# Kernel tuning notes

Hardware: AMD Instinct MI355X
Metric: run time of the kernel (lower is better)

Reference implementation:

```python
import jax, jax.numpy as jnp
import numpy as np

EPS = 1e-8  # torch cosine_similarity clamps norms at 1e-8
TEMPERATURE = 0.05


def _normalize(x):
    n = jnp.linalg.norm(x, axis=-1, keepdims=True)
    return x / jnp.maximum(n, EPS)


def setup_inputs() -> dict:
    key = jax.random.key(0)
    k1, k2, k3 = jax.random.split(key, 3)
    N, D = 8192, 256
    return {
        "text_embeddings": jax.random.normal(k1, (N, D), dtype=jnp.float32),
        "text_pos_embeddings": jax.random.normal(k2, (N, D), dtype=jnp.float32),
        "text_neg_embeddings": jax.random.normal(k3, (N, D), dtype=jnp.float32),
    }


def _pair_loss(a, b):
    # PairInBatchNegCoSentLoss(a, b): cos-sim matrix, scale, diag-subtract, LSE
    sim = _normalize(a) @ _normalize(b).T / TEMPERATURE  # [N, N]
    diff = sim - jnp.diagonal(sim)[:, None]
    return jax.nn.logsumexp(diff, axis=1).mean()


def reference(text_embeddings, text_pos_embeddings, text_neg_embeddings):
    e = _normalize(text_embeddings)
    p = _normalize(text_pos_embeddings)
    n = _normalize(text_neg_embeddings)
    sim_pos = jnp.sum(e * p, axis=-1)          # [N]
    sim_neg = e @ n.T                          # [N, N]
    sim = jnp.concatenate([sim_pos[:, None], sim_neg], axis=1) / TEMPERATURE
    diff = sim - sim[:, 0:1]
    loss = jax.nn.logsumexp(diff, axis=1).mean()
    # add_swap_loss=True: pair loss with (pos, anchor) swapped
    loss = loss + _pair_loss(text_pos_embeddings, text_embeddings)
    return loss
```

## Files before the change

### kernel.cpp

```cpp
#include <hip/hip_runtime.h>
#include <stdint.h>

#define N 8192
#define D 256
#define INV_T 20.0f
#define LOG2E 1.44269504088896340736f
#define BM 128
#define BN 128
#define NXB 64

typedef __attribute__((ext_vector_type(16))) float f32x16;
typedef __attribute__((ext_vector_type(4))) int i32x4;
typedef __attribute__((ext_vector_type(8))) int i32x8;

typedef __attribute__((address_space(3))) uint32_t lds_u32;
typedef __attribute__((address_space(1))) const uint32_t gbl_u32;

static __device__ __forceinline__ float fast_exp2(float x) {
  float r;
  asm("v_exp_f32 %0, %1" : "=v"(r) : "v"(x));
  return r;
}

__global__ __launch_bounds__(256) void normalize_kernel(
    const float* __restrict__ e, const float* __restrict__ p, const float* __restrict__ n,
    uint32_t* __restrict__ eb, uint32_t* __restrict__ pb, uint32_t* __restrict__ nb,
    float* __restrict__ cbuf, float* __restrict__ out) {
  const int tid = threadIdx.x;
  const int wave = tid >> 6, lane = tid & 63;
  const int row = blockIdx.x * 4 + wave;

  if (blockIdx.x == 0 && tid == 0) out[0] = 0.0f;

  const float4 ev = ((const float4*)(e + (size_t)row * D))[lane];
  const float4 pv = ((const float4*)(p + (size_t)row * D))[lane];
  const float4 nv = ((const float4*)(n + (size_t)row * D))[lane];

  float sse = ev.x*ev.x + ev.y*ev.y + ev.z*ev.z + ev.w*ev.w;
  float ssp = pv.x*pv.x + pv.y*pv.y + pv.z*pv.z + pv.w*pv.w;
  float ssn = nv.x*nv.x + nv.y*nv.y + nv.z*nv.z + nv.w*nv.w;
  float dep = ev.x*pv.x + ev.y*pv.y + ev.z*pv.z + ev.w*pv.w;
#pragma unroll
  for (int m = 1; m < 64; m <<= 1) {
    sse += __shfl_xor(sse, m);
    ssp += __shfl_xor(ssp, m);
    ssn += __shfl_xor(ssn, m);
    dep += __shfl_xor(dep, m);
  }
  const float se = 1.0f / fmaxf(sqrtf(sse), 1e-8f);
  const float sp = 1.0f / fmaxf(sqrtf(ssp), 1e-8f);
  const float sn = 1.0f / fmaxf(sqrtf(ssn), 1e-8f);

  int ue = __builtin_amdgcn_cvt_pk_fp8_f32(ev.x*se, ev.y*se, 0, false);
  ue     = __builtin_amdgcn_cvt_pk_fp8_f32(ev.z*se, ev.w*se, ue, true);
  int up = __builtin_amdgcn_cvt_pk_fp8_f32(pv.x*sp, pv.y*sp, 0, false);
  up     = __builtin_amdgcn_cvt_pk_fp8_f32(pv.z*sp, pv.w*sp, up, true);
  int un = __builtin_amdgcn_cvt_pk_fp8_f32(nv.x*sn, nv.y*sn, 0, false);
  un     = __builtin_amdgcn_cvt_pk_fp8_f32(nv.z*sn, nv.w*sn, un, true);
  eb[row * 64 + lane] = (uint32_t)ue;
  pb[row * 64 + lane] = (uint32_t)up;
  nb[row * 64 + lane] = (uint32_t)un;

  if (lane == 0) cbuf[row] = dep * se * sp * INV_T;
}

__global__ __launch_bounds__(256, 3) void simexp_kernel(
    const uint8_t* __restrict__ eb, const uint8_t* __restrict__ pb,
    const uint8_t* __restrict__ nb, const float* __restrict__ cbuf,
    float* __restrict__ part) {
  __shared__ uint8_t Bs[BN * D];

  const int z = blockIdx.z;
  const uint8_t* __restrict__ A = z ? pb : eb;
  const uint8_t* __restrict__ B = z ? eb : nb;

  const int tid = threadIdx.x;
  const int wave = tid >> 6, lane = tid & 63;
  const int lane31 = lane & 31, half = lane >> 5;
  const int rowTile = blockIdx.x * BM, colblk = blockIdx.y;
  const int colTile = colblk * BN;

#pragma unroll
  for (int i = 0; i < 8; ++i) {
    const int c = i * 256 + tid, r = c >> 4, sl = c & 15;
    const int gg = sl ^ (r & 15);
    __builtin_amdgcn_global_load_lds(
        (gbl_u32*)(B + (size_t)(colTile + r) * D + gg * 16),
        (lds_u32*)&Bs[c * 16], 16, 0, 0);
  }

  const int arow = rowTile + wave * 32 + lane31;
  const uint8_t* __restrict__ Arow = A + (size_t)arow * D + half * 32;
  i32x8 afr[4];
#pragma unroll
  for (int s = 0; s < 4; ++s) {
    const i32x4 lo = *(const i32x4*)(Arow + s * 64);
    const i32x4 hi = *(const i32x4*)(Arow + s * 64 + 16);
    afr[s] = (i32x8){lo[0], lo[1], lo[2], lo[3], hi[0], hi[1], hi[2], hi[3]};
  }

  const float cv = cbuf[arow] * LOG2E;

  int bbase[4];
#pragma unroll
  for (int ni = 0; ni < 4; ++ni) {
    const int cl = ni * 32 + lane31;
    bbase[ni] = (cl << 8) ^ ((cl & 15) << 4) ^ (half << 5);
  }

  f32x16 acc[4];
#pragma unroll
  for (int ni = 0; ni < 4; ++ni)
#pragma unroll
    for (int r = 0; r < 16; ++r) acc[ni][r] = 0.0f;

  __syncthreads();

#pragma unroll
  for (int s = 0; s < 4; ++s) {
#pragma unroll
    for (int ni = 0; ni < 4; ++ni) {
      const int alo = bbase[ni] ^ (s << 6);
      const i32x4 blo = *(const i32x4*)&Bs[alo];
      const i32x4 bhi = *(const i32x4*)&Bs[alo ^ 16];
      const i32x8 b = (i32x8){blo[0], blo[1], blo[2], blo[3],
                              bhi[0], bhi[1], bhi[2], bhi[3]};
      acc[ni] = __builtin_amdgcn_mfma_scale_f32_32x32x64_f8f6f4(
          b, afr[s], acc[ni],
          0 , 0 ,
          0, 0x7F7F7F7F , 0, 0x7F7F7F7F );
    }
  }

  const float K2 = INV_T * LOG2E;
  float sacc0 = 0.0f, sacc1 = 0.0f, sacc2 = 0.0f, sacc3 = 0.0f;
#pragma unroll
  for (int reg = 0; reg < 16; ++reg) {
    sacc0 += fast_exp2(acc[0][reg] * K2 - cv);
    sacc1 += fast_exp2(acc[1][reg] * K2 - cv);
    sacc2 += fast_exp2(acc[2][reg] * K2 - cv);
    sacc3 += fast_exp2(acc[3][reg] * K2 - cv);
  }
  float v = (sacc0 + sacc1) + (sacc2 + sacc3);
  v += __shfl_xor(v, 32);
  if (lane < 32)
    part[((size_t)(z * NXB + colblk)) * N + rowTile + wave * 32 + lane] = v;
}

__global__ __launch_bounds__(64) void finalize_kernel(const float* __restrict__ part,
                                                      float* __restrict__ out) {
  const int r = blockIdx.x * 64 + threadIdx.x;
  const int z = r >> 13, row = r & (N - 1);
  const float* __restrict__ base = part + (size_t)(z * NXB) * N + row;
  float s0 = 0.0f, s1 = 0.0f, s2 = 0.0f, s3 = 0.0f;
#pragma unroll
  for (int x = 0; x < NXB; x += 4) {
    s0 += base[(size_t)(x + 0) * N];
    s1 += base[(size_t)(x + 1) * N];
    s2 += base[(size_t)(x + 2) * N];
    s3 += base[(size_t)(x + 3) * N];
  }
  const float s = (s0 + s1) + (s2 + s3);
  float val = z ? logf(s) : log1pf(s);
#pragma unroll
  for (int m = 1; m < 64; m <<= 1) val += __shfl_xor(val, m);
  if (threadIdx.x == 0) atomicAdd(out, val * (1.0f / (float)N));
}

extern "C" void kernel_launch(void* const* d_in, const int* in_sizes, int n_in,
                              void* d_out, int out_size, void* d_ws, size_t ws_size,
                              hipStream_t stream) {
  const float* e = (const float*)d_in[0];
  const float* p = (const float*)d_in[1];
  const float* n = (const float*)d_in[2];

  char* w = (char*)d_ws;
  uint8_t* eb = (uint8_t*)w;
  uint8_t* pb = eb + (size_t)N * D;
  uint8_t* nb = pb + (size_t)N * D;
  float* cbuf = (float*)(nb + (size_t)N * D);
  float* part = cbuf + N;

  normalize_kernel<<<N / 4, 256, 0, stream>>>(e, p, n, (uint32_t*)eb, (uint32_t*)pb,
                                              (uint32_t*)nb, cbuf, (float*)d_out);
  simexp_kernel<<<dim3(N / BM, N / BN, 2), 256, 0, stream>>>(eb, pb, nb, cbuf, part);
  finalize_kernel<<<256, 64, 0, stream>>>(part, (float*)d_out);
}
```

Baseline: 134.1 us.

## Make simexp persistent over column tiles with double-buffered B staging

Each simexp block now keeps its A fragments in registers and loops over 16 consecutive 128-column B tiles. B tiles are double-buffered in LDS via async global-to-LDS loads, so the load of the next-but-one tile overlaps MFMA and exp work. This cuts the grid from 64x64x2 blocks to 4x64x2, amortizes A loads, and shrinks the partial-sum buffer and finalize reduction from 64 to 4 chunks. In exchange it doubles LDS use and lowers the occupancy hint from 3 to 2. The grid drops to 512 blocks, which may underfill the 256 CUs.

```diff
diff --git a/kernel.cpp b/kernel.cpp
--- a/kernel.cpp
+++ b/kernel.cpp
@@ -7,7 +7,8 @@
 #define LOG2E 1.44269504088896340736f
 #define BM 128
 #define BN 128
-#define NXB 64
+#define NCHUNK 4
+#define NT 16
 
 typedef __attribute__((ext_vector_type(16))) float f32x16;
 typedef __attribute__((ext_vector_type(4))) int i32x4;
@@ -64,11 +65,11 @@
   if (lane == 0) cbuf[row] = dep * se * sp * INV_T;
 }
 
-__global__ __launch_bounds__(256, 3) void simexp_kernel(
+__global__ __launch_bounds__(256, 2) void simexp_kernel(
     const uint8_t* __restrict__ eb, const uint8_t* __restrict__ pb,
     const uint8_t* __restrict__ nb, const float* __restrict__ cbuf,
     float* __restrict__ part) {
-  __shared__ uint8_t Bs[BN * D];
+  __shared__ uint8_t Bs[2][BN * D];
 
   const int z = blockIdx.z;
   const uint8_t* __restrict__ A = z ? pb : eb;
@@ -77,17 +78,21 @@
   const int tid = threadIdx.x;
   const int wave = tid >> 6, lane = tid & 63;
   const int lane31 = lane & 31, half = lane >> 5;
-  const int rowTile = blockIdx.x * BM, colblk = blockIdx.y;
-  const int colTile = colblk * BN;
-
-#pragma unroll
-  for (int i = 0; i < 8; ++i) {
-    const int c = i * 256 + tid, r = c >> 4, sl = c & 15;
-    const int gg = sl ^ (r & 15);
-    __builtin_amdgcn_global_load_lds(
-        (gbl_u32*)(B + (size_t)(colTile + r) * D + gg * 16),
-        (lds_u32*)&Bs[c * 16], 16, 0, 0);
-  }
+  const int chunk = blockIdx.x;
+  const int rowTile = blockIdx.y * BM;
+  const int colblk0 = chunk * NT;
+
+#define STAGEB(buf, cblk)                                                     \
+  do {                                                                        \
+    const uint8_t* __restrict__ Bsrc = B + (size_t)(cblk) * (BN * D);         \
+    _Pragma("unroll") for (int i = 0; i < 8; ++i) {                           \
+      const int c = i * 256 + tid, r = c >> 4, sl = c & 15;                   \
+      const int gg = sl ^ (r & 15);                                           \
+      __builtin_amdgcn_global_load_lds(                                       \
+          (gbl_u32*)(Bsrc + (size_t)r * D + gg * 16),                         \
+          (lds_u32*)&Bs[buf][c * 16], 16, 0, 0);                              \
+    }                                                                         \
+  } while (0)
 
   const int arow = rowTile + wave * 32 + lane31;
   const uint8_t* __restrict__ Arow = A + (size_t)arow * D + half * 32;
@@ -98,8 +103,11 @@
     const i32x4 hi = *(const i32x4*)(Arow + s * 64 + 16);
     afr[s] = (i32x8){lo[0], lo[1], lo[2], lo[3], hi[0], hi[1], hi[2], hi[3]};
   }
-
   const float cv = cbuf[arow] * LOG2E;
+  __builtin_amdgcn_sched_barrier(0);
+  STAGEB(0, colblk0 + 0);
+  STAGEB(1, colblk0 + 1);
+  __builtin_amdgcn_sched_barrier(0);
 
   int bbase[4];
 #pragma unroll
@@ -108,58 +116,70 @@
     bbase[ni] = (cl << 8) ^ ((cl & 15) << 4) ^ (half << 5);
   }
 
-  f32x16 acc[4];
-#pragma unroll
-  for (int ni = 0; ni < 4; ++ni)
-#pragma unroll
-    for (int r = 0; r < 16; ++r) acc[ni][r] = 0.0f;
-
-  __syncthreads();
-
-#pragma unroll
-  for (int s = 0; s < 4; ++s) {
-#pragma unroll
-    for (int ni = 0; ni < 4; ++ni) {
-      const int alo = bbase[ni] ^ (s << 6);
-      const i32x4 blo = *(const i32x4*)&Bs[alo];
-      const i32x4 bhi = *(const i32x4*)&Bs[alo ^ 16];
-      const i32x8 b = (i32x8){blo[0], blo[1], blo[2], blo[3],
-                              bhi[0], bhi[1], bhi[2], bhi[3]};
-      acc[ni] = __builtin_amdgcn_mfma_scale_f32_32x32x64_f8f6f4(
-          b, afr[s], acc[ni],
-          0 , 0 ,
-          0, 0x7F7F7F7F , 0, 0x7F7F7F7F );
-    }
-  }
-
   const float K2 = INV_T * LOG2E;
   float sacc0 = 0.0f, sacc1 = 0.0f, sacc2 = 0.0f, sacc3 = 0.0f;
-#pragma unroll
-  for (int reg = 0; reg < 16; ++reg) {
-    sacc0 += fast_exp2(acc[0][reg] * K2 - cv);
-    sacc1 += fast_exp2(acc[1][reg] * K2 - cv);
-    sacc2 += fast_exp2(acc[2][reg] * K2 - cv);
-    sacc3 += fast_exp2(acc[3][reg] * K2 - cv);
-  }
+
+#pragma unroll 1
+  for (int t = 0; t < NT; ++t) {
+    if (t < NT - 1) asm volatile("s_waitcnt vmcnt(8)" ::: "memory");
+    else            asm volatile("s_waitcnt vmcnt(0)" ::: "memory");
+    __builtin_amdgcn_s_barrier();
+    __builtin_amdgcn_sched_barrier(0);
+
+    const int bpar = (t & 1) << 15;
+    f32x16 acc[4];
+#pragma unroll
+    for (int ni = 0; ni < 4; ++ni)
+#pragma unroll
+      for (int r = 0; r < 16; ++r) acc[ni][r] = 0.0f;
+
+#pragma unroll
+    for (int s = 0; s < 4; ++s) {
+#pragma unroll
+      for (int ni = 0; ni < 4; ++ni) {
+        const int alo = (bbase[ni] ^ bpar) ^ (s << 6);
+        const i32x4 blo = *(const i32x4*)&Bs[0][alo];
+        const i32x4 bhi = *(const i32x4*)&Bs[0][alo ^ 16];
+        const i32x8 b = (i32x8){blo[0], blo[1], blo[2], blo[3],
+                                bhi[0], bhi[1], bhi[2], bhi[3]};
+        acc[ni] = __builtin_amdgcn_mfma_scale_f32_32x32x64_f8f6f4(
+            b, afr[s], acc[ni],
+            0 , 0 ,
+            0, 0x7F7F7F7F , 0, 0x7F7F7F7F );
+      }
+    }
+
+    __builtin_amdgcn_sched_barrier(0);
+    __builtin_amdgcn_s_barrier();
+    __builtin_amdgcn_sched_barrier(0);
+
+    if (t + 2 < NT) STAGEB(t & 1, colblk0 + t + 2);
+
+#pragma unroll
+    for (int reg = 0; reg < 16; ++reg) {
+      sacc0 += fast_exp2(acc[0][reg] * K2 - cv);
+      sacc1 += fast_exp2(acc[1][reg] * K2 - cv);
+      sacc2 += fast_exp2(acc[2][reg] * K2 - cv);
+      sacc3 += fast_exp2(acc[3][reg] * K2 - cv);
+    }
+  }
+#undef STAGEB
+
   float v = (sacc0 + sacc1) + (sacc2 + sacc3);
   v += __shfl_xor(v, 32);
   if (lane < 32)
-    part[((size_t)(z * NXB + colblk)) * N + rowTile + wave * 32 + lane] = v;
+    part[((size_t)(z * NCHUNK + chunk)) * N + rowTile + wave * 32 + lane] = v;
 }
 
 __global__ __launch_bounds__(64) void finalize_kernel(const float* __restrict__ part,
                                                       float* __restrict__ out) {
   const int r = blockIdx.x * 64 + threadIdx.x;
   const int z = r >> 13, row = r & (N - 1);
-  const float* __restrict__ base = part + (size_t)(z * NXB) * N + row;
-  float s0 = 0.0f, s1 = 0.0f, s2 = 0.0f, s3 = 0.0f;
-#pragma unroll
-  for (int x = 0; x < NXB; x += 4) {
-    s0 += base[(size_t)(x + 0) * N];
-    s1 += base[(size_t)(x + 1) * N];
-    s2 += base[(size_t)(x + 2) * N];
-    s3 += base[(size_t)(x + 3) * N];
-  }
+  const float* __restrict__ base = part + (size_t)(z * NCHUNK) * N + row;
+  float s0 = base[0];
+  float s1 = base[(size_t)1 * N];
+  float s2 = base[(size_t)2 * N];
+  float s3 = base[(size_t)3 * N];
   const float s = (s0 + s1) + (s2 + s3);
   float val = z ? logf(s) : log1pf(s);
 #pragma unroll
@@ -183,6 +203,6 @@
 
   normalize_kernel<<<N / 4, 256, 0, stream>>>(e, p, n, (uint32_t*)eb, (uint32_t*)pb,
                                               (uint32_t*)nb, cbuf, (float*)d_out);
-  simexp_kernel<<<dim3(N / BM, N / BN, 2), 256, 0, stream>>>(eb, pb, nb, cbuf, part);
+  simexp_kernel<<<dim3(NCHUNK, N / BM, 2), 256, 0, stream>>>(eb, pb, nb, cbuf, part);
   finalize_kernel<<<256, 64, 0, stream>>>(part, (float*)d_out);
 }
```

After: 117.5 us. 1.14x faster.
